# Kernel optimization log

Hardware: AMD Instinct MI355X
Metric: run time of the kernel (lower is better)

## Reference

```python
import jax, jax.numpy as jnp
import numpy as np

B, S, I, O = 64, 512, 256, 256


def setup_inputs() -> dict:
    key = jax.random.key(0)
    ks = jax.random.split(key, 7)
    s_i = 1.0 / np.sqrt(I)
    s_o = 1.0 / np.sqrt(O)
    return {
        "x": jax.random.normal(ks[0], (B, S, I), dtype=jnp.float32),
        "h0": jax.random.normal(ks[1], (B, O), dtype=jnp.float32) * 0.1,
        "c0": jax.random.normal(ks[2], (B, O), dtype=jnp.float32) * 0.1,
        # gate order: [f, i, g, o]; Linear convention y = x @ W.T + b
        "Wh": jax.random.normal(ks[3], (4, O, O), dtype=jnp.float32) * s_o,
        "bh": jax.random.normal(ks[4], (4, O), dtype=jnp.float32) * s_o,
        "Wx": jax.random.normal(ks[5], (4, O, I), dtype=jnp.float32) * s_i,
        "bx": jax.random.normal(ks[6], (4, O), dtype=jnp.float32) * s_i,
    }


def reference(x, h0, c0, Wh, bh, Wx, bx):
    # Precompute all input-side gate projections in one big GEMM: [S, B, 4, O]
    xg = jnp.einsum('bsi,goi->sbgo', x, Wx) + bx + bh  # fold both biases here

    def step(carry, xt):
        h, c = carry
        g = jnp.einsum('bo,gpo->bgp', h, Wh) + xt  # [B, 4, O]
        f = jax.nn.sigmoid(g[:, 0])
        i = jax.nn.sigmoid(g[:, 1])
        gt = jnp.tanh(g[:, 2])
        o = jax.nn.sigmoid(g[:, 3])
        c = c * f + i * gt
        h = o * jnp.tanh(c)
        return (h, c), h

    (hT, cT), hs = jax.lax.scan(step, (h0, c0), xg)
    h_seq = jnp.transpose(hs, (1, 0, 2))  # [B, S, O]
    return h_seq, hT, cT
```

## Files before the change

kernel.cpp:

```cpp
#include <hip/hip_runtime.h>


#define SS 512

typedef _Float16 h2 __attribute__((ext_vector_type(2)));

__device__ __forceinline__ h2 bch(unsigned u) { return __builtin_bit_cast(h2, u); }

__device__ __forceinline__ unsigned rl(unsigned v, int lane) {
  return (unsigned)__builtin_amdgcn_readlane((int)v, lane);
}

#if __has_builtin(__builtin_amdgcn_fdot2)
__device__ __forceinline__ float dot2f(h2 a, h2 b, float c) {
  return __builtin_amdgcn_fdot2(a, b, c, false);
}
#else
__device__ __forceinline__ float dot2f(h2 a, h2 b, float c) {
  return c + (float)a[0] * (float)b[0] + (float)a[1] * (float)b[1];
}
#endif

__device__ __forceinline__ float sigm(float x) { return 1.f / (1.f + __expf(-x)); }
__device__ __forceinline__ float tanh_f(float x) {
  float e = __expf(-2.f * fabsf(x));
  float r = (1.f - e) / (1.f + e);
  return copysignf(r, x);
}

__global__ __launch_bounds__(256) void xg_gemm(
    const float* __restrict__ X, const float* __restrict__ W,
    const float* __restrict__ bx, const float* __restrict__ bh,
    float* __restrict__ out)
{
  __shared__ float As[64][68];
  __shared__ float Bs[64][68];
  const int bm = blockIdx.x >> 4;
  const int bn = blockIdx.x & 15;
  const int tid = threadIdx.x;
  const int tn = tid & 15, tm = tid >> 4;
  const int row0 = bm * 64, col0 = bn * 64;
  float acc[4][4] = {};

  for (int k0 = 0; k0 < 256; k0 += 64) {
#pragma unroll
    for (int i = 0; i < 4; i++) {
      const int m = (tid >> 4) + i * 16;
      const int k = (tid & 15) * 4;
      float4 av = *(const float4*)&X[(size_t)(row0 + m) * 256 + k0 + k];
      *(float4*)&As[m][k] = av;
      float4 wv = *(const float4*)&W[(size_t)(col0 + m) * 256 + k0 + k];
      Bs[k + 0][m] = wv.x; Bs[k + 1][m] = wv.y;
      Bs[k + 2][m] = wv.z; Bs[k + 3][m] = wv.w;
    }
    __syncthreads();
#pragma unroll 8
    for (int kk = 0; kk < 64; kk++) {
      const float a0 = As[tm * 4 + 0][kk];
      const float a1 = As[tm * 4 + 1][kk];
      const float a2 = As[tm * 4 + 2][kk];
      const float a3 = As[tm * 4 + 3][kk];
      const float4 bv = *(const float4*)&Bs[kk][tn * 4];
      acc[0][0] = fmaf(a0, bv.x, acc[0][0]); acc[0][1] = fmaf(a0, bv.y, acc[0][1]);
      acc[0][2] = fmaf(a0, bv.z, acc[0][2]); acc[0][3] = fmaf(a0, bv.w, acc[0][3]);
      acc[1][0] = fmaf(a1, bv.x, acc[1][0]); acc[1][1] = fmaf(a1, bv.y, acc[1][1]);
      acc[1][2] = fmaf(a1, bv.z, acc[1][2]); acc[1][3] = fmaf(a1, bv.w, acc[1][3]);
      acc[2][0] = fmaf(a2, bv.x, acc[2][0]); acc[2][1] = fmaf(a2, bv.y, acc[2][1]);
      acc[2][2] = fmaf(a2, bv.z, acc[2][2]); acc[2][3] = fmaf(a2, bv.w, acc[2][3]);
      acc[3][0] = fmaf(a3, bv.x, acc[3][0]); acc[3][1] = fmaf(a3, bv.y, acc[3][1]);
      acc[3][2] = fmaf(a3, bv.z, acc[3][2]); acc[3][3] = fmaf(a3, bv.w, acc[3][3]);
    }
    __syncthreads();
  }

  float bias[4];
#pragma unroll
  for (int j = 0; j < 4; j++) {
    const int col = col0 + tn * 4 + j;
    bias[j] = bx[col] + bh[col];
  }
#pragma unroll
  for (int i = 0; i < 4; i++) {
    float4 o4;
    o4.x = acc[i][0] + bias[0]; o4.y = acc[i][1] + bias[1];
    o4.z = acc[i][2] + bias[2]; o4.w = acc[i][3] + bias[3];
    *(float4*)&out[(size_t)(row0 + tm * 4 + i) * 1024 + col0 + tn * 4] = o4;
  }
}

__global__ __launch_bounds__(512, 1) void lstm_scan3(
    const float* __restrict__ xg,
    const float* __restrict__ Wh,
    const float* __restrict__ h0,
    const float* __restrict__ c0,
    float* __restrict__ out)
{
  __shared__ __align__(16) _Float16 wl[2 * 8 * 512 * 8];
  __shared__ __align__(16) _Float16 h_sh[256];
  __shared__ float io_i[256];
  __shared__ float io_o[256];

  const int tid = threadIdx.x;
  const int b = blockIdx.x;

  const float* r0 = Wh + (size_t)tid * 256;
  const float* r1 = Wh + (size_t)(tid + 512) * 256;

  h2 w0[96], w1[96];
#pragma unroll
  for (int j = 0; j < 96; ++j) {
    float2 a = *(const float2*)&r0[2 * j];
    float2 c = *(const float2*)&r1[2 * j];
    h2 wa; wa[0] = (_Float16)a.x; wa[1] = (_Float16)a.y; w0[j] = wa;
    h2 wc; wc[0] = (_Float16)c.x; wc[1] = (_Float16)c.y; w1[j] = wc;
  }
#pragma unroll
  for (int c = 0; c < 8; ++c) {
#pragma unroll
    for (int e = 0; e < 8; ++e) {
      wl[((size_t)(c)*512 + tid) * 8 + e]     = (_Float16)r0[192 + c * 8 + e];
      wl[((size_t)(8 + c)*512 + tid) * 8 + e] = (_Float16)r1[192 + c * 8 + e];
    }
  }
  if (tid < 256) h_sh[tid] = (_Float16)h0[(size_t)b * 256 + tid];
  float cr = (tid < 256) ? c0[(size_t)b * 256 + tid] : 0.f;
  __syncthreads();

  const float* xr = xg + (size_t)b * SS * 1024;
  float* hs = out + (size_t)b * SS * 256;

  for (int t = 0; t < SS; ++t) {
    const float xg0 = xr[(size_t)t * 1024 + tid];
    const float xg1 = xr[(size_t)t * 1024 + tid + 512];

    const uint4 hv = *(const uint4*)&h_sh[(tid & 31) * 8];

    float A0 = 0.f, B0 = 0.f, A1 = 0.f, B1 = 0.f;

#pragma unroll
    for (int q = 0; q < 3; ++q) {
#pragma unroll
      for (int g = 0; g < 8; ++g) {
        const int ln = q * 8 + g;
        const unsigned hu0 = rl(hv.x, ln);
        const unsigned hu1 = rl(hv.y, ln);
        const unsigned hu2 = rl(hv.z, ln);
        const unsigned hu3 = rl(hv.w, ln);
        const int j = ln * 4;
        A0 = dot2f(w0[j + 0], bch(hu0), A0); A1 = dot2f(w1[j + 0], bch(hu0), A1);
        B0 = dot2f(w0[j + 1], bch(hu1), B0); B1 = dot2f(w1[j + 1], bch(hu1), B1);
        A0 = dot2f(w0[j + 2], bch(hu2), A0); A1 = dot2f(w1[j + 2], bch(hu2), A1);
        B0 = dot2f(w0[j + 3], bch(hu3), B0); B1 = dot2f(w1[j + 3], bch(hu3), B1);
      }
    }
#pragma unroll
    for (int c = 0; c < 8; ++c) {
      const uint4 wa = *(const uint4*)&wl[((size_t)(c)*512 + tid) * 8];
      const uint4 wb = *(const uint4*)&wl[((size_t)(8 + c)*512 + tid) * 8];
      const int ln = 24 + c;
      const unsigned hu0 = rl(hv.x, ln);
      const unsigned hu1 = rl(hv.y, ln);
      const unsigned hu2 = rl(hv.z, ln);
      const unsigned hu3 = rl(hv.w, ln);
      A0 = dot2f(bch(wa.x), bch(hu0), A0); A1 = dot2f(bch(wb.x), bch(hu0), A1);
      B0 = dot2f(bch(wa.y), bch(hu1), B0); B1 = dot2f(bch(wb.y), bch(hu1), B1);
      A0 = dot2f(bch(wa.z), bch(hu2), A0); A1 = dot2f(bch(wb.z), bch(hu2), A1);
      B0 = dot2f(bch(wa.w), bch(hu3), B0); B1 = dot2f(bch(wb.w), bch(hu3), B1);
    }
    const float y0 = A0 + B0 + xg0;
    const float y1 = A1 + B1 + xg1;

    float u0 = 0.f, u1 = 0.f;
    if (tid < 256) {
      u0 = sigm(y0);
      u1 = tanh_f(y1);
    } else {
      io_i[tid - 256] = sigm(y0);
      io_o[tid - 256] = sigm(y1);
    }
    __syncthreads();

    if (tid < 256) {
      cr = cr * u0 + io_i[tid] * u1;
      const float h = io_o[tid] * tanh_f(cr);
      hs[(size_t)t * 256 + tid] = h;
      h_sh[tid] = (_Float16)h;
      if (t == SS - 1) {
        out[8388608 + (size_t)b * 256 + tid] = h;
        out[8404992 + (size_t)b * 256 + tid] = cr;
      }
    }
    __syncthreads();
  }
}

extern "C" void kernel_launch(void* const* d_in, const int* in_sizes, int n_in,
                              void* d_out, int out_size, void* d_ws, size_t ws_size,
                              hipStream_t stream) {
  const float* x  = (const float*)d_in[0];
  const float* h0 = (const float*)d_in[1];
  const float* c0 = (const float*)d_in[2];
  const float* Wh = (const float*)d_in[3];
  const float* bh = (const float*)d_in[4];
  const float* Wx = (const float*)d_in[5];
  const float* bx = (const float*)d_in[6];
  float* out = (float*)d_out;

  float* xg = (float*)d_ws;

  xg_gemm<<<dim3(8192), dim3(256), 0, stream>>>(x, Wx, bx, bh, xg);
  lstm_scan3<<<dim3(64), dim3(512), 0, stream>>>(xg, Wh, h0, c0, out);
}
```

Measured before the change: 1.284 ms.

## Pair gate rows across adjacent lanes to drop a barrier per LSTM step

Weight rows are remapped so each pair of adjacent lanes holds all four gates of one hidden unit. Gate values are exchanged with a DPP lane swap instead of shared memory, and h is double-buffered, which removes one __syncthreads per timestep. The recurrent dot products now accumulate in packed fp16 FMAs across eight partial sums before a final fp32 reduction. Accumulating in fp16 may lose accuracy, and tanh is computed through sigmoid as 2*sigm(2x)-1.

```diff
diff --git a/kernel.cpp b/kernel.cpp
--- a/kernel.cpp
+++ b/kernel.cpp
@@ -20,6 +20,16 @@
   return c + (float)a[0] * (float)b[0] + (float)a[1] * (float)b[1];
 }
 #endif
+
+__device__ __forceinline__ h2 pkfma(h2 a, h2 b, h2 c) {
+  return __builtin_elementwise_fma(a, b, c);
+}
+
+__device__ __forceinline__ float swap1(float x) {
+  int i = __builtin_bit_cast(int, x);
+  i = __builtin_amdgcn_update_dpp(0, i, 0xB1, 0xF, 0xF, true);
+  return __builtin_bit_cast(float, i);
+}
 
 __device__ __forceinline__ float sigm(float x) { return 1.f / (1.f + __expf(-x)); }
 __device__ __forceinline__ float tanh_f(float x) {
@@ -88,7 +98,7 @@
   }
 }
 
-__global__ __launch_bounds__(512, 1) void lstm_scan3(
+__global__ __launch_bounds__(512) void lstm_scan5(
     const float* __restrict__ xg,
     const float* __restrict__ Wh,
     const float* __restrict__ h0,
@@ -96,15 +106,16 @@
     float* __restrict__ out)
 {
   __shared__ __align__(16) _Float16 wl[2 * 8 * 512 * 8];
-  __shared__ __align__(16) _Float16 h_sh[256];
-  __shared__ float io_i[256];
-  __shared__ float io_o[256];
+  __shared__ __align__(16) _Float16 h_sh[2][256];
 
   const int tid = threadIdx.x;
   const int b = blockIdx.x;
-
-  const float* r0 = Wh + (size_t)tid * 256;
-  const float* r1 = Wh + (size_t)(tid + 512) * 256;
+  const int m = tid >> 1;
+  const int odd = tid & 1;
+  const int row0 = odd * 256 + m;
+
+  const float* r0 = Wh + (size_t)row0 * 256;
+  const float* r1 = Wh + (size_t)(row0 + 512) * 256;
 
   h2 w0[96], w1[96];
 #pragma unroll
@@ -122,36 +133,39 @@
       wl[((size_t)(8 + c)*512 + tid) * 8 + e] = (_Float16)r1[192 + c * 8 + e];
     }
   }
-  if (tid < 256) h_sh[tid] = (_Float16)h0[(size_t)b * 256 + tid];
-  float cr = (tid < 256) ? c0[(size_t)b * 256 + tid] : 0.f;
+  if (tid < 256) h_sh[0][tid] = (_Float16)h0[(size_t)b * 256 + tid];
+  float cr = (!odd) ? c0[(size_t)b * 256 + m] : 0.f;
   __syncthreads();
 
   const float* xr = xg + (size_t)b * SS * 1024;
   float* hs = out + (size_t)b * SS * 256;
 
+  h2 kOne; kOne[0] = (_Float16)1.0f; kOne[1] = (_Float16)1.0f;
+
   for (int t = 0; t < SS; ++t) {
-    const float xg0 = xr[(size_t)t * 1024 + tid];
-    const float xg1 = xr[(size_t)t * 1024 + tid + 512];
-
-    const uint4 hv = *(const uint4*)&h_sh[(tid & 31) * 8];
-
-    float A0 = 0.f, B0 = 0.f, A1 = 0.f, B1 = 0.f;
-
-#pragma unroll
-    for (int q = 0; q < 3; ++q) {
-#pragma unroll
-      for (int g = 0; g < 8; ++g) {
-        const int ln = q * 8 + g;
-        const unsigned hu0 = rl(hv.x, ln);
-        const unsigned hu1 = rl(hv.y, ln);
-        const unsigned hu2 = rl(hv.z, ln);
-        const unsigned hu3 = rl(hv.w, ln);
-        const int j = ln * 4;
-        A0 = dot2f(w0[j + 0], bch(hu0), A0); A1 = dot2f(w1[j + 0], bch(hu0), A1);
-        B0 = dot2f(w0[j + 1], bch(hu1), B0); B1 = dot2f(w1[j + 1], bch(hu1), B1);
-        A0 = dot2f(w0[j + 2], bch(hu2), A0); A1 = dot2f(w1[j + 2], bch(hu2), A1);
-        B0 = dot2f(w0[j + 3], bch(hu3), B0); B1 = dot2f(w1[j + 3], bch(hu3), B1);
-      }
+    const int p = t & 1;
+    const float xg0 = xr[(size_t)t * 1024 + row0];
+    const float xg1 = xr[(size_t)t * 1024 + row0 + 512];
+
+    const uint4 hv = *(const uint4*)&h_sh[p][(tid & 31) * 8];
+
+    h2 pA[8] = {}, pB[8] = {};
+
+#pragma unroll
+    for (int ln = 0; ln < 24; ++ln) {
+      const unsigned hu0 = rl(hv.x, ln);
+      const unsigned hu1 = rl(hv.y, ln);
+      const unsigned hu2 = rl(hv.z, ln);
+      const unsigned hu3 = rl(hv.w, ln);
+      const int j = ln * 4;
+      pA[(j + 0) & 7] = pkfma(w0[j + 0], bch(hu0), pA[(j + 0) & 7]);
+      pB[(j + 0) & 7] = pkfma(w1[j + 0], bch(hu0), pB[(j + 0) & 7]);
+      pA[(j + 1) & 7] = pkfma(w0[j + 1], bch(hu1), pA[(j + 1) & 7]);
+      pB[(j + 1) & 7] = pkfma(w1[j + 1], bch(hu1), pB[(j + 1) & 7]);
+      pA[(j + 2) & 7] = pkfma(w0[j + 2], bch(hu2), pA[(j + 2) & 7]);
+      pB[(j + 2) & 7] = pkfma(w1[j + 2], bch(hu2), pB[(j + 2) & 7]);
+      pA[(j + 3) & 7] = pkfma(w0[j + 3], bch(hu3), pA[(j + 3) & 7]);
+      pB[(j + 3) & 7] = pkfma(w1[j + 3], bch(hu3), pB[(j + 3) & 7]);
     }
 #pragma unroll
     for (int c = 0; c < 8; ++c) {
@@ -162,32 +176,39 @@
       const unsigned hu1 = rl(hv.y, ln);
       const unsigned hu2 = rl(hv.z, ln);
       const unsigned hu3 = rl(hv.w, ln);
-      A0 = dot2f(bch(wa.x), bch(hu0), A0); A1 = dot2f(bch(wb.x), bch(hu0), A1);
-      B0 = dot2f(bch(wa.y), bch(hu1), B0); B1 = dot2f(bch(wb.y), bch(hu1), B1);
-      A0 = dot2f(bch(wa.z), bch(hu2), A0); A1 = dot2f(bch(wb.z), bch(hu2), A1);
-      B0 = dot2f(bch(wa.w), bch(hu3), B0); B1 = dot2f(bch(wb.w), bch(hu3), B1);
-    }
-    const float y0 = A0 + B0 + xg0;
-    const float y1 = A1 + B1 + xg1;
-
-    float u0 = 0.f, u1 = 0.f;
-    if (tid < 256) {
-      u0 = sigm(y0);
-      u1 = tanh_f(y1);
-    } else {
-      io_i[tid - 256] = sigm(y0);
-      io_o[tid - 256] = sigm(y1);
-    }
-    __syncthreads();
-
-    if (tid < 256) {
-      cr = cr * u0 + io_i[tid] * u1;
-      const float h = io_o[tid] * tanh_f(cr);
-      hs[(size_t)t * 256 + tid] = h;
-      h_sh[tid] = (_Float16)h;
+      const int j = c * 4;
+      pA[(j + 0) & 7] = pkfma(bch(wa.x), bch(hu0), pA[(j + 0) & 7]);
+      pB[(j + 0) & 7] = pkfma(bch(wb.x), bch(hu0), pB[(j + 0) & 7]);
+      pA[(j + 1) & 7] = pkfma(bch(wa.y), bch(hu1), pA[(j + 1) & 7]);
+      pB[(j + 1) & 7] = pkfma(bch(wb.y), bch(hu1), pB[(j + 1) & 7]);
+      pA[(j + 2) & 7] = pkfma(bch(wa.z), bch(hu2), pA[(j + 2) & 7]);
+      pB[(j + 2) & 7] = pkfma(bch(wb.z), bch(hu2), pB[(j + 2) & 7]);
+      pA[(j + 3) & 7] = pkfma(bch(wa.w), bch(hu3), pA[(j + 3) & 7]);
+      pB[(j + 3) & 7] = pkfma(bch(wb.w), bch(hu3), pB[(j + 3) & 7]);
+    }
+    float y0 = xg0, y1 = xg1;
+#pragma unroll
+    for (int c = 0; c < 8; ++c) {
+      y0 = dot2f(pA[c], kOne, y0);
+      y1 = dot2f(pB[c], kOne, y1);
+    }
+
+    const float u0 = sigm(y0);
+    const float z  = odd ? y1 : 2.f * y1;
+    const float sz = sigm(z);
+    const float u1 = odd ? sz : 2.f * sz - 1.f;
+
+    const float v0 = swap1(u0);
+    const float v1 = swap1(u1);
+
+    if (!odd) {
+      cr = cr * u0 + v0 * u1;
+      const float h = v1 * tanh_f(cr);
+      hs[(size_t)t * 256 + m] = h;
+      h_sh[p ^ 1][m] = (_Float16)h;
       if (t == SS - 1) {
-        out[8388608 + (size_t)b * 256 + tid] = h;
-        out[8404992 + (size_t)b * 256 + tid] = cr;
+        out[8388608 + (size_t)b * 256 + m] = h;
+        out[8404992 + (size_t)b * 256 + m] = cr;
       }
     }
     __syncthreads();
@@ -209,5 +230,5 @@
   float* xg = (float*)d_ws;
 
   xg_gemm<<<dim3(8192), dim3(256), 0, stream>>>(x, Wx, bx, bh, xg);
-  lstm_scan3<<<dim3(64), dim3(512), 0, stream>>>(xg, Wh, h0, c0, out);
-}
+  lstm_scan5<<<dim3(64), dim3(512), 0, stream>>>(xg, Wh, h0, c0, out);
+}
```

Measured after the change: 1.274 ms. Within noise of the previous version (-0.8%).
